# Performance work log

Measured on AMD Instinct MI355X. Metric: run time of the kernel, lower is better.

Reference implementation:

```python
import jax, jax.numpy as jnp
import numpy as np

E, H, LQ, LC, B = 1024, 16, 1024, 512, 4
HD = E // H
FF = 4 * E
EPS = 1e-6


def _rope(x):
    # x: [B, H, L, D]; interleaved rotary embedding (lucidrains-style)
    D, L = x.shape[-1], x.shape[-2]
    inv_freq = 1.0 / (10000.0 ** (jnp.arange(0, D, 2, dtype=jnp.float32) / D))
    ang = jnp.arange(L, dtype=jnp.float32)[:, None] * inv_freq[None, :]  # [L, D/2]
    cos, sin = jnp.cos(ang), jnp.sin(ang)
    x1, x2 = x[..., 0::2], x[..., 1::2]
    r1 = x1 * cos - x2 * sin
    r2 = x1 * sin + x2 * cos
    return jnp.stack([r1, r2], axis=-1).reshape(x.shape)


def _ln(x, w, b):
    mu = jnp.mean(x, -1, keepdims=True)
    var = jnp.mean(jnp.square(x - mu), -1, keepdims=True)
    return (x - mu) * jax.lax.rsqrt(var + EPS) * w + b


def _rope_attn(x, ctx, qw, qb, kw, kb, vw, vb, pw, pb, mask):
    Bn, L, Em = x.shape
    Lc = ctx.shape[1]
    q = (x @ qw.T + qb).reshape(Bn, L, H, HD).transpose(0, 2, 1, 3)
    k = (ctx @ kw.T + kb).reshape(Bn, Lc, H, HD).transpose(0, 2, 1, 3)
    v = (ctx @ vw.T + vb).reshape(Bn, Lc, H, HD).transpose(0, 2, 1, 3)
    q, k = _rope(q), _rope(k)
    s = jnp.einsum('bhic,bhjc->bhij', q, k) / np.sqrt(HD).astype(np.float32)
    if mask is not None:
        s = jnp.where(mask[None, None], -jnp.inf, s)
    p = jax.nn.softmax(s, axis=-1)
    o = jnp.einsum('bhij,bhjc->bhic', p, v)
    o = o.transpose(0, 2, 1, 3).reshape(Bn, L, Em)
    return o @ pw.T + pb


def setup_inputs() -> dict:
    key = jax.random.key(0)
    ks = iter(jax.random.split(key, 40))
    s = 0.02
    d = {}
    d['x'] = jax.random.normal(next(ks), (B, LQ, E), jnp.float32)
    d['context'] = jax.random.normal(next(ks), (B, LC, E), jnp.float32)
    d['attn_mask'] = jnp.triu(jnp.ones((LQ, LQ), bool), k=1)  # True = masked (causal)
    for g in ('g_msa', 'g_ca', 'g_mlp'):
        d[g] = jax.random.normal(next(ks), (1, 1, E), jnp.float32) * s
    for n in ('n1', 'n2', 'n3'):
        d[n + '_w'] = jnp.ones((E,), jnp.float32)
        d[n + '_b'] = jnp.zeros((E,), jnp.float32)
    for p in ('sa', 'ca'):
        for m in ('q', 'k', 'v', 'p'):
            d[f'{p}_{m}w'] = jax.random.normal(next(ks), (E, E), jnp.float32) * s
            d[f'{p}_{m}b'] = jnp.zeros((E,), jnp.float32)
    d['fc1_w'] = jax.random.normal(next(ks), (FF, E), jnp.float32) * s
    d['fc1_b'] = jnp.zeros((FF,), jnp.float32)
    d['fc2_w'] = jax.random.normal(next(ks), (E, FF), jnp.float32) * s
    d['fc2_b'] = jnp.zeros((E,), jnp.float32)
    return d


def reference(x, context, attn_mask,
              g_msa, g_ca, g_mlp,
              n1_w, n1_b, n2_w, n2_b, n3_w, n3_b,
              sa_qw, sa_qb, sa_kw, sa_kb, sa_vw, sa_vb, sa_pw, sa_pb,
              ca_qw, ca_qb, ca_kw, ca_kb, ca_vw, ca_vb, ca_pw, ca_pb,
              fc1_w, fc1_b, fc2_w, fc2_b):
    # self-attention (causal RoPE) with zero-init learned gate
    x = x + g_msa * _rope_attn(_ln(x, n1_w, n1_b), _ln(x, n1_w, n1_b),
                               sa_qw, sa_qb, sa_kw, sa_kb, sa_vw, sa_vb,
                               sa_pw, sa_pb, attn_mask)
    # cross-attention (RoPE on both streams, no mask)
    h = _ln(x, n2_w, n2_b)
    x = x + g_ca * _rope_attn(h, context,
                              ca_qw, ca_qb, ca_kw, ca_kb, ca_vw, ca_vb,
                              ca_pw, ca_pb, None)
    # gated MLP with tanh-approx GELU
    h = _ln(x, n3_w, n3_b)
    h = jax.nn.gelu(h @ fc1_w.T + fc1_b, approximate=True) @ fc2_w.T + fc2_b
    x = x + g_mlp * h
    return x
```

## Files before the change

kernel.cpp:

```cpp
#include <hip/hip_runtime.h>
#include <math.h>

#if !__has_builtin(__builtin_amdgcn_cvt_pk_fp8_f32)
#include <hip/hip_fp8.h>
#endif

typedef __attribute__((ext_vector_type(8))) short short8;
typedef __attribute__((ext_vector_type(4))) float f32x4;
typedef __attribute__((ext_vector_type(16))) float f32x16;
typedef unsigned char u8;
typedef unsigned short u16;
typedef unsigned int u32;
typedef __attribute__((ext_vector_type(2))) u32 u32x2;
typedef __attribute__((ext_vector_type(4))) u32 u32x4;
typedef __attribute__((ext_vector_type(8))) int i32x8;
typedef unsigned long long u64;

static constexpr int E = 1024, H = 16, LQ = 1024, LC = 512, Bn = 4, FF = 4096;
static constexpr int NTOK = Bn * LQ;
static constexpr int NCTX = Bn * LC;

#define QSCALE 0.1803368801111244f
#define DEFER_THR 11.5f
#define AOSCL 16.0f

static constexpr size_t OFF_TCOS   = 0;
static constexpr size_t OFF_TSIN   = OFF_TCOS + (size_t)LQ*32*4;
static constexpr size_t OFF_BSAQKV = OFF_TSIN + (size_t)LQ*32*4;
static constexpr size_t OFF_BCAKV  = OFF_BSAQKV + 16384;
static constexpr size_t OFF_W8     = OFF_BCAKV + 16384;
static constexpr size_t OFF_W8QKV  = OFF_W8;
static constexpr size_t OFF_W8SAP  = OFF_W8QKV  + (size_t)3*1048576;
static constexpr size_t OFF_W8CAQ  = OFF_W8SAP  + (size_t)1*1048576;
static constexpr size_t OFF_W8CAKV = OFF_W8CAQ  + (size_t)1*1048576;
static constexpr size_t OFF_W8CAP  = OFF_W8CAKV + (size_t)2*1048576;
static constexpr size_t OFF_W8FC1  = OFF_W8CAP  + (size_t)1*1048576;
static constexpr size_t OFF_W8FC2  = OFF_W8FC1  + (size_t)4*1048576;
static constexpr size_t OFF_CTX8   = OFF_W8FC2  + (size_t)4*1048576;
static constexpr size_t OFF_CTXB   = OFF_W8 + (size_t)30*1048576 + (size_t)2048*1024*2;
static constexpr size_t OFF_H      = OFF_CTXB   + (size_t)2048*1024*2;
static constexpr size_t OFF_QKV    = OFF_H      + (size_t)4096*1024*2;
static constexpr size_t OFF_CAQ    = OFF_QKV;
static constexpr size_t OFF_CAKV   = OFF_QKV + (size_t)4096*1024*2;
static constexpr size_t OFF_QR     = OFF_QKV + (size_t)4096*3072*2;
static constexpr size_t OFF_KR     = OFF_QR  + (size_t)4096*1024*2;
static constexpr size_t OFF_VT     = OFF_KR  + (size_t)4096*1024*2;
static constexpr size_t OFF_AO     = OFF_VT  + (size_t)4096*1024*2;
static constexpr size_t OFF_U      = OFF_QKV;
static constexpr size_t WS_NEED    = OFF_AO + (size_t)4096*1024*2;

static __device__ __forceinline__ float bf2f(u16 u) {
  union { u32 i; float f; } un; un.i = ((u32)u) << 16; return un.f;
}
static __device__ __forceinline__ u16 f2bf(float f) {
  union { float f; u32 u; } un; un.f = f;
  u32 u = un.u;
  return (u16)((u + 0x7FFFu + ((u >> 16) & 1u)) >> 16);
}
static __device__ __forceinline__ u64 pack4(u16 a, u16 b, u16 c, u16 d) {
  return (u64)a | ((u64)b << 16) | ((u64)c << 32) | ((u64)d << 48);
}
static __device__ __forceinline__ f32x16 mfma32(short8 a, short8 b, f32x16 c) {
  return __builtin_amdgcn_mfma_f32_32x32x16_bf16(a, b, c, 0, 0, 0);
}
static __device__ __forceinline__ void gload_lds16(void* lds, const void* g) {
  __builtin_amdgcn_global_load_lds(
      (const __attribute__((address_space(1))) void*)g,
      (__attribute__((address_space(3))) void*)lds, 16, 0, 0);
}
static __device__ __forceinline__ float gelu_tanh(float x) {
  float z2 = 1.5957691216057308f * (x + 0.044715f * x * x * x);
  float e = __expf(z2);
  float r = __builtin_amdgcn_rcpf(e + 1.0f);
  return x - x * r;
}
static __device__ __forceinline__ u32 cvtpk_bf16(float lo, float hi) {
  u32 r;
  asm("v_cvt_pk_bf16_f32 %0, %1, %2" : "=v"(r) : "v"(lo), "v"(hi));
  return r;
}
static __device__ __forceinline__ u32 pack_fp8x4(float a, float b, float c, float d) {
#if __has_builtin(__builtin_amdgcn_cvt_pk_fp8_f32)
  u32 r = (u32)__builtin_amdgcn_cvt_pk_fp8_f32(a, b, 0, false);
  r = (u32)__builtin_amdgcn_cvt_pk_fp8_f32(c, d, (int)r, true);
  return r;
#else
  __hip_fp8_e4m3 qa(a), qb(b), qc(c), qd(d);
  return (u32)qa.__x | ((u32)qb.__x << 8) | ((u32)qc.__x << 16) | ((u32)qd.__x << 24);
#endif
}
static __device__ __forceinline__ u8 fp8b(float f) {
#if __has_builtin(__builtin_amdgcn_cvt_pk_fp8_f32)
  return (u8)((u32)__builtin_amdgcn_cvt_pk_fp8_f32(f, f, 0, false) & 0xFFu);
#else
  __hip_fp8_e4m3 t(f); return t.__x;
#endif
}

__global__ __launch_bounds__(256) void build_tab(float* __restrict__ ct, float* __restrict__ st) {
  int idx = blockIdx.x * 256 + threadIdx.x;
  int pos = idx >> 5, i = idx & 31;
  float inv = powf(10000.f, -(float)i * (1.f / 32.f));
  float a = (float)pos * inv;
  ct[idx] = cosf(a);
  st[idx] = sinf(a);
}

struct CvtF8 { const float* s[10]; };
__global__ __launch_bounds__(256) void cvt_fp8c(CvtF8 a, const float* __restrict__ ctx,
                                                u8* __restrict__ dst) {
  u32 gid = blockIdx.x * 256 + threadIdx.x;
  u32 seg = gid >> 18, off = gid & 262143u;
  const float* s;
  float scl = 256.f;
  if (seg < 8)       s = a.s[seg];
  else if (seg < 12) s = a.s[8] + (size_t)(seg - 8) * 1048576;
  else if (seg < 16) s = a.s[9] + (size_t)(seg - 12) * 1048576;
  else             { s = ctx + (size_t)(seg - 16) * 1048576; scl = 16.f; }
  float4 v = *(const float4*)(s + (size_t)off * 4);
  *(u32*)(dst + (size_t)seg * 1048576 + (size_t)off * 4) =
      pack_fp8x4(v.x * scl, v.y * scl, v.z * scl, v.w * scl);
}

struct Cp5 { const float* s[5]; };
__global__ __launch_bounds__(256) void copy5(Cp5 a, float* __restrict__ dst) {
  int gid = blockIdx.x * 256 + threadIdx.x;
  int s = gid >> 10, off = gid & 1023;
  int doff = (s < 3) ? s * 1024 : 4096 + (s - 3) * 1024;
  dst[doff + off] = a.s[s][off];
}

__global__ __launch_bounds__(256) void init_bias_gate(float* __restrict__ out, const float* __restrict__ bias,
                                                      const float* __restrict__ gate) {
  int i = (blockIdx.x * 256 + threadIdx.x) * 4;
  int c = i & 1023;
  float4 o = *(float4*)(out + i);
  o.x += gate[c] * bias[c];
  o.y += gate[c + 1] * bias[c + 1];
  o.z += gate[c + 2] * bias[c + 2];
  o.w += gate[c + 3] * bias[c + 3];
  *(float4*)(out + i) = o;
}

__global__ __launch_bounds__(256) void ln_fp8(const float* __restrict__ x, const float* __restrict__ w,
                                              const float* __restrict__ b, u8* __restrict__ out) {
  __shared__ float red[4];
  int row = blockIdx.x, tid = threadIdx.x;
  const float* xr = x + (size_t)row * 1024;
  float4 v = ((const float4*)xr)[tid];
  float s = v.x + v.y + v.z + v.w;
#pragma unroll
  for (int off = 32; off; off >>= 1) s += __shfl_xor(s, off);
  if ((tid & 63) == 0) red[tid >> 6] = s;
  __syncthreads();
  float mean = (red[0] + red[1] + red[2] + red[3]) * (1.f / 1024.f);
  float dx = v.x - mean, dy = v.y - mean, dz = v.z - mean, dw = v.w - mean;
  float sq = dx * dx + dy * dy + dz * dz + dw * dw;
#pragma unroll
  for (int off = 32; off; off >>= 1) sq += __shfl_xor(sq, off);
  __syncthreads();
  if ((tid & 63) == 0) red[tid >> 6] = sq;
  __syncthreads();
  float var = (red[0] + red[1] + red[2] + red[3]) * (1.f / 1024.f);
  float rstd = rsqrtf(var + 1e-6f);
  float4 wv = ((const float4*)w)[tid];
  float4 bv = ((const float4*)b)[tid];
  u32 pk = pack_fp8x4((dx * rstd * wv.x + bv.x) * 16.f, (dy * rstd * wv.y + bv.y) * 16.f,
                      (dz * rstd * wv.z + bv.z) * 16.f, (dw * rstd * wv.w + bv.w) * 16.f);
  *(u32*)(out + (size_t)row * 1024 + tid * 4) = pk;
}

struct RopeJob { const u16* src; u16* dst; int ld, col0, Lper, T; float scale; };
struct Rope2 { RopeJob j[2]; };
__global__ __launch_bounds__(128) void rope2(Rope2 a, const float* __restrict__ cosT,
                                             const float* __restrict__ sinT) {
  RopeJob jb = a.j[blockIdx.y];
  int t = blockIdx.x;
  if (t >= jb.T) return;
  int b = t / jb.Lper, l = t - b * jb.Lper;
  int tid = threadIdx.x;
  int e0 = tid * 8;
  int h = e0 >> 6, d0 = e0 & 63;
  short8 vv = *(const short8*)(jb.src + (size_t)t * jb.ld + jb.col0 + e0);
  short8 ov;
#pragma unroll
  for (int j = 0; j < 4; ++j) {
    float x1 = bf2f((u16)vv[2 * j]);
    float x2 = bf2f((u16)vv[2 * j + 1]);
    int i = (d0 >> 1) + j;
    float c = cosT[l * 32 + i], s = sinT[l * 32 + i];
    ov[2 * j]     = (short)f2bf((x1 * c - x2 * s) * jb.scale);
    ov[2 * j + 1] = (short)f2bf((x1 * s + x2 * c) * jb.scale);
  }
  *(short8*)(jb.dst + (((size_t)b * H + h) * jb.Lper + l) * 64 + d0) = ov;
}

__global__ __launch_bounds__(256) void vtrans(const u16* __restrict__ src, int ld, int col0,
                                              u16* __restrict__ dst, int Lper) {
  __shared__ u16 tile[64][72];
  int bh = blockIdx.y;
  int b = bh >> 4, h = bh & 15;
  int l0 = blockIdx.x * 64;
  int tid = threadIdx.x;
#pragma unroll
  for (int j = 0; j < 2; ++j) {
    int c = tid + j * 256;
    int i = c >> 3, d0 = (c & 7) * 8;
    short8 v = *(const short8*)(src + (size_t)(b * Lper + l0 + i) * ld + col0 + h * 64 + d0);
    *(short8*)(&tile[i][d0]) = v;
  }
  __syncthreads();
#pragma unroll
  for (int j = 0; j < 2; ++j) {
    int c = tid + j * 256;
    int d = c >> 3, lc = (c & 7) * 8;
    short8 v;
#pragma unroll
    for (int k = 0; k < 8; ++k) v[k] = (short)tile[lc + k][d];
    *(short8*)(dst + (((size_t)bh) * 64 + d) * Lper + l0 + lc) = v;
  }
}

enum { E8_BF16 = 0, E8_GELU = 1, E8_ATOMIC = 2, E8_RESID = 3 };

template <int EPI>
__global__ __launch_bounds__(256, 2) void gemm8(const u8* __restrict__ A, const u8* __restrict__ W,
                                                const float* __restrict__ bias, u16* outb16,
                                                u8* outb8, float* outf, const float* res,
                                                const float* __restrict__ gate,
                                                int M, int N, int K, int kchunks) {
  __shared__ u8 As[2][128 * 128];
  __shared__ u8 Bs[2][128 * 128];

  int nwg = gridDim.x * gridDim.y;
  int bid = blockIdx.y * gridDim.x + blockIdx.x;
  int cpx = nwg >> 3;
  int swz = (bid & 7) * cpx + (bid >> 3);
  int bx = swz % gridDim.x, by = swz / gridDim.x;
  int row0 = by * 128, col0 = bx * 128;

  const int Kc = K / kchunks;
  const int kbase = blockIdx.z * Kc;

  int tid = threadIdx.x;
  int lane = tid & 63, wid = tid >> 6;
  int wr = wid >> 1, wc = wid & 1;
  int lr = lane & 15, lg = lane >> 4;

  u32 aoff[4], boff[4];
  int ldso[4];
#pragma unroll
  for (int j = 0; j < 4; ++j) {
    int q = tid + j * 256;
    int r = q >> 3, p = q & 7, sp = p ^ (r & 7);
    aoff[j] = (u32)(row0 + r) * (u32)K + sp * 16;
    boff[j] = (u32)(col0 + r) * (u32)K + sp * 16;
    ldso[j] = q * 16;
  }

  f32x4 acc[4][4] = {};
  const int nkt = Kc >> 7;

  auto rdfrag = [&](const u8* base, int r, i32x8& f) {
    const u8* rp = base + r * 128;
    int ck = lg * 2;
    u32x4 lo = *(const u32x4*)(rp + ((ck) ^ (r & 7)) * 16);
    u32x4 hh = *(const u32x4*)(rp + ((ck + 1) ^ (r & 7)) * 16);
    i32x8 v;
    v[0] = (int)lo[0]; v[1] = (int)lo[1]; v[2] = (int)lo[2]; v[3] = (int)lo[3];
    v[4] = (int)hh[0]; v[5] = (int)hh[1]; v[6] = (int)hh[2]; v[7] = (int)hh[3];
    f = v;
  };

#pragma unroll
  for (int j = 0; j < 4; ++j) {
    gload_lds16(&As[0][ldso[j]], A + aoff[j] + kbase);
    gload_lds16(&Bs[0][ldso[j]], W + boff[j] + kbase);
  }
  __syncthreads();

  for (int kt = 0; kt < nkt; ++kt) {
    int cur = kt & 1;
    if (kt + 1 < nkt) {
      int k0 = kbase + ((kt + 1) << 7);
#pragma unroll
      for (int j = 0; j < 4; ++j) {
        gload_lds16(&As[cur ^ 1][ldso[j]], A + aoff[j] + k0);
        gload_lds16(&Bs[cur ^ 1][ldso[j]], W + boff[j] + k0);
      }
    }
    i32x8 a[4], b[4];
#pragma unroll
    for (int m = 0; m < 4; ++m) rdfrag(&As[cur][0], wr * 64 + m * 16 + lr, a[m]);
#pragma unroll
    for (int n = 0; n < 4; ++n) rdfrag(&Bs[cur][0], wc * 64 + n * 16 + lr, b[n]);
    __builtin_amdgcn_s_setprio(1);
#pragma unroll
    for (int m = 0; m < 4; ++m)
#pragma unroll
      for (int n = 0; n < 4; ++n)
        acc[m][n] = __builtin_amdgcn_mfma_scale_f32_16x16x128_f8f6f4(
            a[m], b[n], acc[m][n], 0, 0, 0, 0x7F7F7F7F, 0, 0x7F7F7F7F);
    __builtin_amdgcn_s_setprio(0);
    __syncthreads();
  }

  constexpr float SCL = 1.f / 4096.f;
  if (EPI == E8_BF16) {
    u16* Ct = (u16*)&As[0][0];
#pragma unroll
    for (int n = 0; n < 4; ++n) {
      int cl = wc * 64 + n * 16 + lr;
      float bv = bias[col0 + cl];
#pragma unroll
      for (int m = 0; m < 4; ++m) {
#pragma unroll
        for (int i = 0; i < 4; ++i) {
          int rl = wr * 64 + m * 16 + lg * 4 + i;
          Ct[rl * 128 + cl] = f2bf(acc[m][n][i] * SCL + bv);
        }
      }
    }
    __syncthreads();
#pragma unroll
    for (int j = 0; j < 8; ++j) {
      u32 q = (u32)tid + j * 256;
      u32 r = q >> 4, ck = q & 15;
      short8 v = *(const short8*)(Ct + r * 128 + ck * 8);
      *(short8*)(outb16 + (size_t)(row0 + r) * N + col0 + ck * 8) = v;
    }
  } else if (EPI == E8_GELU) {
    u8* Ct = &As[0][0];
#pragma unroll
    for (int n = 0; n < 4; ++n) {
      int cl = wc * 64 + n * 16 + lr;
      float bv = bias[col0 + cl];
#pragma unroll
      for (int m = 0; m < 4; ++m) {
#pragma unroll
        for (int i = 0; i < 4; ++i) {
          int rl = wr * 64 + m * 16 + lg * 4 + i;
          float v = acc[m][n][i] * SCL + bv;
          Ct[rl * 128 + cl] = fp8b(gelu_tanh(v) * 16.f);
        }
      }
    }
    __syncthreads();
#pragma unroll
    for (int j = 0; j < 4; ++j) {
      int q = tid + j * 256;
      int r = q >> 3, ck = q & 7;
      *(u32x4*)(outb8 + (size_t)(row0 + r) * N + col0 + ck * 16) =
          *(const u32x4*)(Ct + r * 128 + ck * 16);
    }
  } else if (EPI == E8_RESID) {
#pragma unroll
    for (int n = 0; n < 4; ++n) {
      int cg = col0 + wc * 64 + n * 16 + lr;
      float bv = bias[cg], gv = gate[cg];
#pragma unroll
      for (int m = 0; m < 4; ++m) {
#pragma unroll
        for (int i = 0; i < 4; ++i) {
          int rg = row0 + wr * 64 + m * 16 + lg * 4 + i;
          float v = acc[m][n][i] * SCL + bv;
          float r = res[(size_t)rg * N + cg];
          outf[(size_t)rg * N + cg] = r + gv * v;
        }
      }
    }
  } else {
#pragma unroll
    for (int n = 0; n < 4; ++n) {
      int cg = col0 + wc * 64 + n * 16 + lr;
      float gv = gate[cg];
#pragma unroll
      for (int m = 0; m < 4; ++m) {
#pragma unroll
        for (int i = 0; i < 4; ++i) {
          int rg = row0 + wr * 64 + m * 16 + lg * 4 + i;
          atomicAdd(&outf[(size_t)rg * N + cg], gv * (acc[m][n][i] * SCL));
        }
      }
    }
  }
}

template <int MASKED, int PRE>
static __device__ __forceinline__ void attn_tile3(short8* kf, const u16* KtNext,
                                                  const u16* Vp0, const u16* Vp1,
                                                  const short8* qf, int kb, int q0, int l31, int hi,
                                                  float& m, float& lsum, f32x16& o0, f32x16& o1) {
  short8 vf0[4], vf1[4];
#pragma unroll
  for (int ks = 0; ks < 4; ++ks) {
    vf0[ks] = *(const short8*)(Vp0 + ks * 16 + hi * 8);
    vf1[ks] = *(const short8*)(Vp1 + ks * 16 + hi * 8);
  }
  f32x16 s0 = {}, s1 = {};
  __builtin_amdgcn_s_setprio(1);
#pragma unroll
  for (int s = 0; s < 4; ++s) {
    s0 = mfma32(kf[s], qf[s], s0);
    s1 = mfma32(kf[4 + s], qf[s], s1);
  }
  __builtin_amdgcn_s_setprio(0);
  if (PRE) {
    const u16* kp0 = KtNext + (size_t)l31 * 64 + hi * 8;
    const u16* kp1 = KtNext + (size_t)(32 + l31) * 64 + hi * 8;
#pragma unroll
    for (int s = 0; s < 4; ++s) {
      kf[s] = *(const short8*)(kp0 + s * 16);
      kf[4 + s] = *(const short8*)(kp1 + s * 16);
    }
  }
  if (MASKED) {
    int qg = q0 + l31;
#pragma unroll
    for (int r = 0; r < 16; ++r) {
      int kk = kb + (r & 3) + 8 * (r >> 2) + 4 * hi;
      if (kk > qg) s0[r] = -INFINITY;
      if (kk + 32 > qg) s1[r] = -INFINITY;
    }
  }
  float pm = -INFINITY;
#pragma unroll
  for (int r = 0; r < 16; ++r) pm = fmaxf(pm, fmaxf(s0[r], s1[r]));
  pm = fmaxf(pm, __shfl_xor(pm, 32));
  if (!__all(pm <= m + DEFER_THR)) {
    float mn = fmaxf(m, pm);
    float al = exp2f(m - mn);
    m = mn;
    lsum *= al;
#pragma unroll
    for (int r = 0; r < 16; ++r) {
      float alr = __shfl(al, (r & 3) + 8 * (r >> 2) + 4 * hi);
      o0[r] *= alr;
      o1[r] *= alr;
    }
  }
  float ts = 0.f;
#pragma unroll
  for (int r = 0; r < 16; ++r) {
    float p0 = exp2f(s0[r] - m);
    float p1 = exp2f(s1[r] - m);
    s0[r] = p0; s1[r] = p1;
    ts += p0 + p1;
  }
  ts += __shfl_xor(ts, 32);
  lsum += ts;
  auto pack8 = [&](float a0, float a1, float a2, float a3,
                   float a4, float a5, float a6, float a7) -> short8 {
    u32 c0 = cvtpk_bf16(a0, a1), c1 = cvtpk_bf16(a2, a3);
    u32 c2 = cvtpk_bf16(a4, a5), c3 = cvtpk_bf16(a6, a7);
    u32x2 r02 = __builtin_amdgcn_permlane32_swap(c0, c2, false, false);
    u32x2 r13 = __builtin_amdgcn_permlane32_swap(c1, c3, false, false);
    u32x4 w;
    w[0] = r02[0]; w[1] = r13[0]; w[2] = r02[1]; w[3] = r13[1];
    return __builtin_bit_cast(short8, w);
  };
  short8 pa0 = pack8(s0[0], s0[1], s0[2], s0[3], s0[4], s0[5], s0[6], s0[7]);
  short8 pa1 = pack8(s0[8], s0[9], s0[10], s0[11], s0[12], s0[13], s0[14], s0[15]);
  short8 pa2 = pack8(s1[0], s1[1], s1[2], s1[3], s1[4], s1[5], s1[6], s1[7]);
  short8 pa3 = pack8(s1[8], s1[9], s1[10], s1[11], s1[12], s1[13], s1[14], s1[15]);
  short8 pa[4] = {pa0, pa1, pa2, pa3};
  __builtin_amdgcn_s_setprio(1);
#pragma unroll
  for (int ks = 0; ks < 4; ++ks) {
    o0 = mfma32(pa[ks], vf0[ks], o0);
    o1 = mfma32(pa[ks], vf1[ks], o1);
  }
  __builtin_amdgcn_s_setprio(0);
}

template <int CAUSAL>
__global__ __launch_bounds__(256) void flash_attn2(const u16* __restrict__ Q, const u16* __restrict__ K,
                                                   const u16* __restrict__ Vt, u8* __restrict__ O,
                                                   int Lq, int Lk) {
  const int wid = threadIdx.x >> 6, lane = threadIdx.x & 63;
  const int l31 = lane & 31, hi = lane >> 5;
  int wg = blockIdx.x * 4 + wid;
  int bh = wg & 63;
  int qc = wg >> 6;
  if (CAUSAL) qc = (Lq >> 5) - 1 - qc;
  int q0 = qc << 5;

  const u16* Qb = Q + ((size_t)bh * Lq + q0) * 64;
  const u16* Kb = K + (size_t)bh * Lk * 64;
  const u16* Vb = Vt + (size_t)bh * 64 * Lk;

  short8 qf[4];
#pragma unroll
  for (int s = 0; s < 4; ++s) qf[s] = *(const short8*)(Qb + (size_t)l31 * 64 + s * 16 + hi * 8);

  f32x16 o0 = {}, o1 = {};
  float m = -INFINITY, lsum = 0.f;

  const u16* Kt = Kb;
  const u16* Vp0 = Vb + (size_t)l31 * Lk;
  const u16* Vp1 = Vb + (size_t)(32 + l31) * Lk;

  short8 kf[8];
  {
    const u16* kp0 = Kt + (size_t)l31 * 64 + hi * 8;
    const u16* kp1 = Kt + (size_t)(32 + l31) * 64 + hi * 8;
#pragma unroll
    for (int s = 0; s < 4; ++s) {
      kf[s] = *(const short8*)(kp0 + s * 16);
      kf[4 + s] = *(const short8*)(kp1 + s * 16);
    }
  }

  int nt = CAUSAL ? ((q0 >> 6) + 1) : (Lk >> 6);
  for (int t = 0; t < nt - 1; ++t) {
    attn_tile3<0, 1>(kf, Kt + 64 * 64, Vp0, Vp1, qf, t * 64, q0, l31, hi, m, lsum, o0, o1);
    Kt += 64 * 64; Vp0 += 64; Vp1 += 64;
  }
  if (CAUSAL)
    attn_tile3<1, 0>(kf, nullptr, Vp0, Vp1, qf, (nt - 1) * 64, q0, l31, hi, m, lsum, o0, o1);
  else
    attn_tile3<0, 0>(kf, nullptr, Vp0, Vp1, qf, (nt - 1) * 64, q0, l31, hi, m, lsum, o0, o1);

  float myinv = AOSCL / lsum;
  int b = bh >> 4, h = bh & 15;
#pragma unroll
  for (int r = 0; r < 16; ++r) {
    int cr = (r & 3) + 8 * (r >> 2) + 4 * hi;
    float li = __shfl(myinv, cr);
    u8* op = O + ((size_t)b * Lq + q0 + cr) * 1024 + h * 64;
    op[l31] = fp8b(o0[r] * li);
    op[32 + l31] = fp8b(o1[r] * li);
  }
}

extern "C" void kernel_launch(void* const* d_in, const int* in_sizes, int n_in,
                              void* d_out, int out_size, void* d_ws, size_t ws_size,
                              hipStream_t stream) {
  (void)in_sizes; (void)n_in; (void)out_size;
  if (ws_size < WS_NEED) return;

  const float* x     = (const float*)d_in[0];
  const float* ctx   = (const float*)d_in[1];
  const float* g_msa = (const float*)d_in[3];
  const float* g_ca  = (const float*)d_in[4];
  const float* g_mlp = (const float*)d_in[5];
  const float* n1w = (const float*)d_in[6],  *n1b = (const float*)d_in[7];
  const float* n2w = (const float*)d_in[8],  *n2b = (const float*)d_in[9];
  const float* n3w = (const float*)d_in[10], *n3b = (const float*)d_in[11];
  const float* sa_qw = (const float*)d_in[12], *sa_kw = (const float*)d_in[14];
  const float* sa_vw = (const float*)d_in[16], *sa_pw = (const float*)d_in[18];
  const float* sa_qb = (const float*)d_in[13], *sa_kb = (const float*)d_in[15];
  const float* sa_vb = (const float*)d_in[17], *sa_pb = (const float*)d_in[19];
  const float* ca_qw = (const float*)d_in[20], *ca_qb = (const float*)d_in[21];
  const float* ca_kw = (const float*)d_in[22], *ca_kb = (const float*)d_in[23];
  const float* ca_vw = (const float*)d_in[24], *ca_vb = (const float*)d_in[25];
  const float* ca_pw = (const float*)d_in[26], *ca_pb = (const float*)d_in[27];
  const float* fc1w = (const float*)d_in[28], *fc1b = (const float*)d_in[29];
  const float* fc2w = (const float*)d_in[30], *fc2b = (const float*)d_in[31];

  char* ws = (char*)d_ws;
  float* out = (float*)d_out;
  float* tcos = (float*)(ws + OFF_TCOS);
  float* tsin = (float*)(ws + OFF_TSIN);
  u16* QKV  = (u16*)(ws + OFF_QKV);
  u16* QR   = (u16*)(ws + OFF_QR);
  u16* KR   = (u16*)(ws + OFF_KR);
  u16* VT   = (u16*)(ws + OFF_VT);
  u8*  AO8  = (u8*)(ws + OFF_AO);
  u8*  H8   = (u8*)(ws + OFF_H);
  u8*  U8   = (u8*)(ws + OFF_U);
  u8*  W8QKV  = (u8*)(ws + OFF_W8QKV);
  u8*  W8SAP  = (u8*)(ws + OFF_W8SAP);
  u8*  W8CAQ  = (u8*)(ws + OFF_W8CAQ);
  u8*  W8CAKV = (u8*)(ws + OFF_W8CAKV);
  u8*  W8CAP  = (u8*)(ws + OFF_W8CAP);
  u8*  W8FC1  = (u8*)(ws + OFF_W8FC1);
  u8*  W8FC2  = (u8*)(ws + OFF_W8FC2);
  u8*  CTX8   = (u8*)(ws + OFF_CTX8);

  build_tab<<<dim3(128), dim3(256), 0, stream>>>(tcos, tsin);
  CvtF8 cf;
  cf.s[0] = sa_qw; cf.s[1] = sa_kw; cf.s[2] = sa_vw; cf.s[3] = sa_pw;
  cf.s[4] = ca_qw; cf.s[5] = ca_kw; cf.s[6] = ca_vw; cf.s[7] = ca_pw;
  cf.s[8] = fc1w;  cf.s[9] = fc2w;
  cvt_fp8c<<<dim3(18432), dim3(256), 0, stream>>>(cf, ctx, W8QKV);
  Cp5 cp;
  cp.s[0] = sa_qb; cp.s[1] = sa_kb; cp.s[2] = sa_vb; cp.s[3] = ca_kb; cp.s[4] = ca_vb;
  copy5<<<dim3(20), dim3(256), 0, stream>>>(cp, (float*)(ws + OFF_BSAQKV));

  ln_fp8<<<dim3(NTOK), dim3(256), 0, stream>>>(x, n1w, n1b, H8);
  gemm8<E8_BF16><<<dim3(3072 / 128, NTOK / 128), dim3(256), 0, stream>>>(
      H8, W8QKV, (float*)(ws + OFF_BSAQKV), QKV, nullptr, nullptr, nullptr, nullptr,
      NTOK, 3072, 1024, 1);
  {
    Rope2 r;
    r.j[0] = {QKV, QR, 3072, 0,    LQ, NTOK, QSCALE};
    r.j[1] = {QKV, KR, 3072, 1024, LQ, NTOK, 1.0f};
    rope2<<<dim3(NTOK, 2), dim3(128), 0, stream>>>(r, tcos, tsin);
  }
  vtrans<<<dim3(LQ / 64, Bn * H), dim3(256), 0, stream>>>(QKV, 3072, 2048, VT, LQ);
  flash_attn2<1><<<dim3(512), dim3(256), 0, stream>>>(QR, KR, VT, AO8, LQ, LQ);
  gemm8<E8_RESID><<<dim3(1024 / 128, NTOK / 128), dim3(256), 0, stream>>>(
      AO8, W8SAP, sa_pb, nullptr, nullptr, out, x, g_msa, NTOK, 1024, 1024, 1);

  ln_fp8<<<dim3(NTOK), dim3(256), 0, stream>>>(out, n2w, n2b, H8);
  gemm8<E8_BF16><<<dim3(1024 / 128, NTOK / 128), dim3(256), 0, stream>>>(
      H8, W8CAQ, ca_qb, (u16*)(ws + OFF_CAQ), nullptr, nullptr, nullptr, nullptr,
      NTOK, 1024, 1024, 1);
  gemm8<E8_BF16><<<dim3(2048 / 128, NCTX / 128), dim3(256), 0, stream>>>(
      CTX8, W8CAKV, (float*)(ws + OFF_BCAKV), (u16*)(ws + OFF_CAKV), nullptr, nullptr,
      nullptr, nullptr, NCTX, 2048, 1024, 1);
  {
    Rope2 r;
    r.j[0] = {(u16*)(ws + OFF_CAQ),  QR, 1024, 0, LQ, NTOK, QSCALE};
    r.j[1] = {(u16*)(ws + OFF_CAKV), KR, 2048, 0, LC, NCTX, 1.0f};
    rope2<<<dim3(NTOK, 2), dim3(128), 0, stream>>>(r, tcos, tsin);
  }
  vtrans<<<dim3(LC / 64, Bn * H), dim3(256), 0, stream>>>(
      (u16*)(ws + OFF_CAKV), 2048, 1024, VT, LC);
  flash_attn2<0><<<dim3(512), dim3(256), 0, stream>>>(QR, KR, VT, AO8, LQ, LC);
  gemm8<E8_RESID><<<dim3(1024 / 128, NTOK / 128), dim3(256), 0, stream>>>(
      AO8, W8CAP, ca_pb, nullptr, nullptr, out, out, g_ca, NTOK, 1024, 1024, 1);

  ln_fp8<<<dim3(NTOK), dim3(256), 0, stream>>>(out, n3w, n3b, H8);
  gemm8<E8_GELU><<<dim3(4096 / 128, NTOK / 128), dim3(256), 0, stream>>>(
      H8, W8FC1, fc1b, nullptr, U8, nullptr, nullptr, nullptr, NTOK, 4096, 1024, 1);
  init_bias_gate<<<dim3(4096), dim3(256), 0, stream>>>(out, fc2b, g_mlp);
  gemm8<E8_ATOMIC><<<dim3(1024 / 128, NTOK / 128, 2), dim3(256), 0, stream>>>(
      U8, W8FC2, nullptr, nullptr, nullptr, out, nullptr, g_mlp, NTOK, 1024, 4096, 2);
}
```

Before: 312.8 us.

## Load GEMM A fragments directly from global memory, drop A LDS staging

The fp8 GEMM no longer stages the A tile through shared memory; each wave reads its A fragments straight from global memory per k-step, while B stays double-buffered in LDS. This halves LDS usage, and launch bounds are raised to allow three blocks per CU. The FC2 split-K factor is doubled to four. The risk is exposed global-load latency on A with no prefetch, plus duplicated A reads across waves, and more atomic traffic on the FC2 output.

```diff
diff --git a/kernel.cpp b/kernel.cpp
--- a/kernel.cpp
+++ b/kernel.cpp
@@ -224,12 +224,11 @@
 enum { E8_BF16 = 0, E8_GELU = 1, E8_ATOMIC = 2, E8_RESID = 3 };
 
 template <int EPI>
-__global__ __launch_bounds__(256, 2) void gemm8(const u8* __restrict__ A, const u8* __restrict__ W,
+__global__ __launch_bounds__(256, 3) void gemm8(const u8* __restrict__ A, const u8* __restrict__ W,
                                                 const float* __restrict__ bias, u16* outb16,
                                                 u8* outb8, float* outf, const float* res,
                                                 const float* __restrict__ gate,
                                                 int M, int N, int K, int kchunks) {
-  __shared__ u8 As[2][128 * 128];
   __shared__ u8 Bs[2][128 * 128];
 
   int nwg = gridDim.x * gridDim.y;
@@ -247,21 +246,33 @@
   int wr = wid >> 1, wc = wid & 1;
   int lr = lane & 15, lg = lane >> 4;
 
-  u32 aoff[4], boff[4];
+  u32 boff[4];
   int ldso[4];
 #pragma unroll
   for (int j = 0; j < 4; ++j) {
     int q = tid + j * 256;
     int r = q >> 3, p = q & 7, sp = p ^ (r & 7);
-    aoff[j] = (u32)(row0 + r) * (u32)K + sp * 16;
     boff[j] = (u32)(col0 + r) * (u32)K + sp * 16;
     ldso[j] = q * 16;
   }
+  const u8* arow[4];
+#pragma unroll
+  for (int m = 0; m < 4; ++m)
+    arow[m] = A + (size_t)(row0 + wr * 64 + m * 16 + lr) * K + lg * 32 + kbase;
 
   f32x4 acc[4][4] = {};
   const int nkt = Kc >> 7;
 
-  auto rdfrag = [&](const u8* base, int r, i32x8& f) {
+  auto rdA = [&](int m, int kb, i32x8& f) {
+    const u8* rp = arow[m] + kb;
+    u32x4 lo = *(const u32x4*)(rp);
+    u32x4 hh = *(const u32x4*)(rp + 16);
+    i32x8 v;
+    v[0] = (int)lo[0]; v[1] = (int)lo[1]; v[2] = (int)lo[2]; v[3] = (int)lo[3];
+    v[4] = (int)hh[0]; v[5] = (int)hh[1]; v[6] = (int)hh[2]; v[7] = (int)hh[3];
+    f = v;
+  };
+  auto rdB = [&](const u8* base, int r, i32x8& f) {
     const u8* rp = base + r * 128;
     int ck = lg * 2;
     u32x4 lo = *(const u32x4*)(rp + ((ck) ^ (r & 7)) * 16);
@@ -273,10 +284,7 @@
   };
 
 #pragma unroll
-  for (int j = 0; j < 4; ++j) {
-    gload_lds16(&As[0][ldso[j]], A + aoff[j] + kbase);
-    gload_lds16(&Bs[0][ldso[j]], W + boff[j] + kbase);
-  }
+  for (int j = 0; j < 4; ++j) gload_lds16(&Bs[0][ldso[j]], W + boff[j] + kbase);
   __syncthreads();
 
   for (int kt = 0; kt < nkt; ++kt) {
@@ -284,16 +292,13 @@
     if (kt + 1 < nkt) {
       int k0 = kbase + ((kt + 1) << 7);
 #pragma unroll
-      for (int j = 0; j < 4; ++j) {
-        gload_lds16(&As[cur ^ 1][ldso[j]], A + aoff[j] + k0);
-        gload_lds16(&Bs[cur ^ 1][ldso[j]], W + boff[j] + k0);
-      }
+      for (int j = 0; j < 4; ++j) gload_lds16(&Bs[cur ^ 1][ldso[j]], W + boff[j] + k0);
     }
     i32x8 a[4], b[4];
 #pragma unroll
-    for (int m = 0; m < 4; ++m) rdfrag(&As[cur][0], wr * 64 + m * 16 + lr, a[m]);
-#pragma unroll
-    for (int n = 0; n < 4; ++n) rdfrag(&Bs[cur][0], wc * 64 + n * 16 + lr, b[n]);
+    for (int m = 0; m < 4; ++m) rdA(m, kt << 7, a[m]);
+#pragma unroll
+    for (int n = 0; n < 4; ++n) rdB(&Bs[cur][0], wc * 64 + n * 16 + lr, b[n]);
     __builtin_amdgcn_s_setprio(1);
 #pragma unroll
     for (int m = 0; m < 4; ++m)
@@ -307,7 +312,7 @@
 
   constexpr float SCL = 1.f / 4096.f;
   if (EPI == E8_BF16) {
-    u16* Ct = (u16*)&As[0][0];
+    u16* Ct = (u16*)&Bs[0][0];
 #pragma unroll
     for (int n = 0; n < 4; ++n) {
       int cl = wc * 64 + n * 16 + lr;
@@ -330,7 +335,7 @@
       *(short8*)(outb16 + (size_t)(row0 + r) * N + col0 + ck * 8) = v;
     }
   } else if (EPI == E8_GELU) {
-    u8* Ct = &As[0][0];
+    u8* Ct = &Bs[0][0];
 #pragma unroll
     for (int n = 0; n < 4; ++n) {
       int cl = wc * 64 + n * 16 + lr;
@@ -626,6 +631,6 @@
   gemm8<E8_GELU><<<dim3(4096 / 128, NTOK / 128), dim3(256), 0, stream>>>(
       H8, W8FC1, fc1b, nullptr, U8, nullptr, nullptr, nullptr, NTOK, 4096, 1024, 1);
   init_bias_gate<<<dim3(4096), dim3(256), 0, stream>>>(out, fc2b, g_mlp);
-  gemm8<E8_ATOMIC><<<dim3(1024 / 128, NTOK / 128, 2), dim3(256), 0, stream>>>(
-      U8, W8FC2, nullptr, nullptr, nullptr, out, nullptr, g_mlp, NTOK, 1024, 4096, 2);
-}
+  gemm8<E8_ATOMIC><<<dim3(1024 / 128, NTOK / 128, 4), dim3(256), 0, stream>>>(
+      U8, W8FC2, nullptr, nullptr, nullptr, out, nullptr, g_mlp, NTOK, 1024, 4096, 4);
+}
```

Result: slower. 381.6 us (+22.0%).
